# Performance work log

Hardware: AMD Instinct MI355X
Metric: run time of the kernel (lower is better)

## Reference

```python
import jax, jax.numpy as jnp
from jax import lax
import numpy as np


def setup_inputs() -> dict:
    key = jax.random.key(0)
    kx, = jax.random.split(key, 1)
    B, T = 4096, 4096
    x = jax.random.normal(kx, (B, T), dtype=jnp.float32)
    omega_log = jnp.asarray(0.0, dtype=jnp.float32)
    alpha_log = jnp.asarray(0.0, dtype=jnp.float32)
    beta_log = jnp.asarray(0.0, dtype=jnp.float32)
    return {"x": x, "omega_log": omega_log, "alpha_log": alpha_log, "beta_log": beta_log}


def reference(x, omega_log, alpha_log, beta_log):
    # x: [B, T]
    ea = jnp.exp(alpha_log)
    eb = jnp.exp(beta_log)
    denom = 1.0 + ea + eb
    omega = jnp.exp(omega_log)
    alpha = ea / denom
    beta = eb / denom

    # initial variance: unbiased sample variance over time (torch.var default ddof=1)
    s0 = jnp.var(x, axis=1, ddof=1)  # [B]

    xsq = jnp.swapaxes(x[:, :-1] ** 2, 0, 1)  # [T-1, B]

    def step(s_prev, x2_t):
        s_t = omega + alpha * x2_t + beta * s_prev
        return s_t, s_t

    _, rest = lax.scan(step, s0, xsq)  # rest: [T-1, B]
    sigma2 = jnp.concatenate([s0[None, :], rest], axis=0)  # [T, B]
    return jnp.sqrt(jnp.swapaxes(sigma2, 0, 1))  # [B, T]
```

## Files before the change

### kernel.cpp

```cpp
#include <hip/hip_runtime.h>
#include <math.h>

#define B_ROWS 4096
#define T_COLS 4096
#define NTHREADS 256
#define WPB 4
#define NBLOCKS (B_ROWS / WPB)
#define NSTRIPE 16

__device__ __forceinline__ float rfl(float v) {
    return __int_as_float(__builtin_amdgcn_readfirstlane(__float_as_int(v)));
}

#define STEP(z, xv) fmaf(beta, (z), fmaf(alpha, (xv) * (xv), omega))
#define SQ(z) __builtin_amdgcn_sqrtf(z)

__global__ __launch_bounds__(NTHREADS, 4) void garch_fused(
    const float* __restrict__ x,
    const float* __restrict__ p_omega_log,
    const float* __restrict__ p_alpha_log,
    const float* __restrict__ p_beta_log,
    float* __restrict__ out)
{
    const int lane = threadIdx.x & 63;
    const int wv   = threadIdx.x >> 6;
    const long row = (long)blockIdx.x * WPB + wv;

    const float4* X4 = reinterpret_cast<const float4*>(x + row * T_COLS);
    float4*       O4 = reinterpret_cast<float4*>(out + row * T_COLS);

    float ea_p  = expf(p_alpha_log[0]);
    float eb_p  = expf(p_beta_log[0]);
    float denom = 1.0f + ea_p + eb_p;
    float omega = rfl(expf(p_omega_log[0]));
    float alpha = rfl(ea_p / denom);
    float beta  = rfl(eb_p / denom);
    float beta2 = beta * beta;
    float beta3 = beta2 * beta;
    float beta4 = beta2 * beta2;

    float sum = 0.0f, ssq = 0.0f;
#pragma unroll
    for (int s = 0; s < NSTRIPE; ++s) {
        float4 a = X4[64 * s + lane];
        sum += (a.x + a.y) + (a.z + a.w);
        ssq = fmaf(a.x, a.x, ssq); ssq = fmaf(a.y, a.y, ssq);
        ssq = fmaf(a.z, a.z, ssq); ssq = fmaf(a.w, a.w, ssq);
    }
#pragma unroll
    for (int d = 32; d > 0; d >>= 1) {
        sum += __shfl_xor(sum, d);
        ssq += __shfl_xor(ssq, d);
    }
    float s0 = (ssq - sum * sum * (1.0f / T_COLS)) * (1.0f / (T_COLS - 1));
    s0 = fmaxf(s0, 0.0f);

    float E = s0;
    float carryX = 0.0f;
    float4 a = X4[lane];
#pragma unroll
    for (int s = 0; s < NSTRIPE; ++s) {
        float4 an = a;
        if (s + 1 < NSTRIPE) an = X4[64 * (s + 1) + lane];

        float xm1 = __shfl_up(a.w, 1);
        if (lane == 0) xm1 = carryX;

        float ia, ib;
        if (s == 0 && lane == 0) {
            float zb = fmaf(alpha, a.x * a.x, omega);
            zb = STEP(zb, a.y); zb = STEP(zb, a.z);
            ia = beta3; ib = zb;
        } else {
            float zb = fmaf(alpha, xm1 * xm1, omega);
            zb = STEP(zb, a.x); zb = STEP(zb, a.y); zb = STEP(zb, a.z);
            ia = beta4; ib = zb;
        }

#pragma unroll
        for (int d = 1; d < 64; d <<= 1) {
            float pa = __shfl_up(ia, d);
            float pb = __shfl_up(ib, d);
            if (lane >= d) { ib = fmaf(ia, pb, ib); ia = ia * pa; }
        }

        float pea = __shfl_up(ia, 1);
        float peb = __shfl_up(ib, 1);
        if (lane == 0) { pea = 1.0f; peb = 0.0f; }
        float e = fmaf(pea, E, peb);

        float4 q;
        float z;
        if (s == 0 && lane == 0) { z = e; }
        else                     { z = STEP(e, xm1); }
        q.x = SQ(z);
        z = STEP(z, a.x); q.y = SQ(z);
        z = STEP(z, a.y); q.z = SQ(z);
        z = STEP(z, a.z); q.w = SQ(z);
        O4[64 * s + lane] = q;

        float ia63 = __shfl(ia, 63);
        float ib63 = __shfl(ib, 63);
        E = fmaf(ia63, E, ib63);
        carryX = __shfl(a.w, 63);
        a = an;
    }
}

extern "C" void kernel_launch(void* const* d_in, const int* in_sizes, int n_in,
                              void* d_out, int out_size, void* d_ws, size_t ws_size,
                              hipStream_t stream) {
    const float* x         = (const float*)d_in[0];
    const float* omega_log = (const float*)d_in[1];
    const float* alpha_log = (const float*)d_in[2];
    const float* beta_log  = (const float*)d_in[3];
    float* out = (float*)d_out;

    garch_fused<<<NBLOCKS, NTHREADS, 0, stream>>>(x, omega_log, alpha_log, beta_log, out);
}
```

Before: 121.6 us.

## Process 8 elements per lane and precompute constant-coefficient scan multipliers

Each lane now handles two float4 chunks (8 timesteps) per stripe, halving the number of stripes and cross-lane scans. Because the recurrence's multiplicative coefficient is a constant power of beta, the scan now carries only the additive part and uses precomputed beta powers, removing half the shuffles and the multiplies. The per-lane prefix multiplier is built once from lane bits. This lengthens each lane's serial chain and adds register use, and large powers of beta may underflow, though that matches the exact math.

```diff
diff --git a/kernel.cpp b/kernel.cpp
--- a/kernel.cpp
+++ b/kernel.cpp
@@ -6,7 +6,7 @@
 #define NTHREADS 256
 #define WPB 4
 #define NBLOCKS (B_ROWS / WPB)
-#define NSTRIPE 16
+#define NSTRIPE 8
 
 __device__ __forceinline__ float rfl(float v) {
     return __int_as_float(__builtin_amdgcn_readfirstlane(__float_as_int(v)));
@@ -35,13 +35,29 @@
     float omega = rfl(expf(p_omega_log[0]));
     float alpha = rfl(ea_p / denom);
     float beta  = rfl(eb_p / denom);
+
     float beta2 = beta * beta;
-    float beta3 = beta2 * beta;
     float beta4 = beta2 * beta2;
+    float beta7 = beta4 * beta2 * beta;
+    float c1  = beta4 * beta4;
+    float c2  = c1  * c1;
+    float c4  = c2  * c2;
+    float c8  = c4  * c4;
+    float c16 = c8  * c8;
+    float c32 = c16 * c16;
+
+    float blA = (lane & 1)  ? c1  : 1.0f;
+    if (lane & 2)  blA *= c2;
+    if (lane & 4)  blA *= c4;
+    if (lane & 8)  blA *= c8;
+    if (lane & 16) blA *= c16;
+    if (lane & 32) blA *= c32;
+    const float Anorm = blA * c1;
+    const float Azero = blA * beta7;
 
     float sum = 0.0f, ssq = 0.0f;
 #pragma unroll
-    for (int s = 0; s < NSTRIPE; ++s) {
+    for (int s = 0; s < 16; ++s) {
         float4 a = X4[64 * s + lane];
         sum += (a.x + a.y) + (a.z + a.w);
         ssq = fmaf(a.x, a.x, ssq); ssq = fmaf(a.y, a.y, ssq);
@@ -57,53 +73,60 @@
 
     float E = s0;
     float carryX = 0.0f;
-    float4 a = X4[lane];
+    float4 a = X4[2 * lane];
+    float4 b = X4[2 * lane + 1];
 #pragma unroll
     for (int s = 0; s < NSTRIPE; ++s) {
-        float4 an = a;
-        if (s + 1 < NSTRIPE) an = X4[64 * (s + 1) + lane];
+        float4 an, bn;
+        if (s + 1 < NSTRIPE) {
+            const float4* Xn = X4 + 128 * (s + 1) + 2 * lane;
+            an = Xn[0];
+            bn = Xn[1];
+        } else {
+            an = a; bn = b;
+        }
 
-        float xm1 = __shfl_up(a.w, 1);
+        float xm1 = __shfl_up(b.w, 1);
         if (lane == 0) xm1 = carryX;
 
-        float ia, ib;
-        if (s == 0 && lane == 0) {
-            float zb = fmaf(alpha, a.x * a.x, omega);
-            zb = STEP(zb, a.y); zb = STEP(zb, a.z);
-            ia = beta3; ib = zb;
-        } else {
-            float zb = fmaf(alpha, xm1 * xm1, omega);
-            zb = STEP(zb, a.x); zb = STEP(zb, a.y); zb = STEP(zb, a.z);
-            ia = beta4; ib = zb;
-        }
+        float z0 = (s == 0 && lane == 0) ? fmaf(alpha, a.x * a.x, omega)
+                                         : STEP(fmaf(alpha, xm1 * xm1, omega), a.x);
+        z0 = STEP(z0, a.y); z0 = STEP(z0, a.z); z0 = STEP(z0, a.w);
+        z0 = STEP(z0, b.x); z0 = STEP(z0, b.y); z0 = STEP(z0, b.z);
+        float ib = z0;
 
-#pragma unroll
-        for (int d = 1; d < 64; d <<= 1) {
-            float pa = __shfl_up(ia, d);
-            float pb = __shfl_up(ib, d);
-            if (lane >= d) { ib = fmaf(ia, pb, ib); ia = ia * pa; }
-        }
+        float pb;
+        pb = __shfl_up(ib, 1);  if (lane >= 1)  ib = fmaf(c1,  pb, ib);
+        pb = __shfl_up(ib, 2);  if (lane >= 2)  ib = fmaf(c2,  pb, ib);
+        pb = __shfl_up(ib, 4);  if (lane >= 4)  ib = fmaf(c4,  pb, ib);
+        pb = __shfl_up(ib, 8);  if (lane >= 8)  ib = fmaf(c8,  pb, ib);
+        pb = __shfl_up(ib, 16); if (lane >= 16) ib = fmaf(c16, pb, ib);
+        pb = __shfl_up(ib, 32); if (lane >= 32) ib = fmaf(c32, pb, ib);
 
-        float pea = __shfl_up(ia, 1);
-        float peb = __shfl_up(ib, 1);
-        if (lane == 0) { pea = 1.0f; peb = 0.0f; }
-        float e = fmaf(pea, E, peb);
+        float A  = (s == 0) ? Azero : Anorm;
+        float ex = fmaf(A, E, ib);
+        float e  = __shfl_up(ex, 1);
+        if (lane == 0) e = E;
+        float Enext = __shfl(ex, 63);
+        float carryN = __shfl(b.w, 63);
 
-        float4 q;
-        float z;
-        if (s == 0 && lane == 0) { z = e; }
-        else                     { z = STEP(e, xm1); }
-        q.x = SQ(z);
-        z = STEP(z, a.x); q.y = SQ(z);
-        z = STEP(z, a.y); q.z = SQ(z);
-        z = STEP(z, a.z); q.w = SQ(z);
-        O4[64 * s + lane] = q;
+        float4 q1, q2;
+        float z = (s == 0 && lane == 0) ? e : STEP(e, xm1);
+        q1.x = SQ(z);
+        z = STEP(z, a.x); q1.y = SQ(z);
+        z = STEP(z, a.y); q1.z = SQ(z);
+        z = STEP(z, a.z); q1.w = SQ(z);
+        z = STEP(z, a.w); q2.x = SQ(z);
+        z = STEP(z, b.x); q2.y = SQ(z);
+        z = STEP(z, b.y); q2.z = SQ(z);
+        z = STEP(z, b.z); q2.w = SQ(z);
+        float4* On = O4 + 128 * s + 2 * lane;
+        On[0] = q1;
+        On[1] = q2;
 
-        float ia63 = __shfl(ia, 63);
-        float ib63 = __shfl(ib, 63);
-        E = fmaf(ia63, E, ib63);
-        carryX = __shfl(a.w, 63);
-        a = an;
+        carryX = carryN;
+        E = Enext;
+        a = an; b = bn;
     }
 }
 
```

New measurement: 127.0 us. 1.04x slower.
